# Kernel tuning notes

Measured on AMD Instinct MI355X. Metric: run time of the kernel, lower is better.

## Reference

```python
import jax, jax.numpy as jnp
import numpy as np

E = 800000
NUM_RADIAL = 6
HIDDEN = 128
OUT = 128
NUM_NODES = 50000


def setup_inputs() -> dict:
    key = jax.random.key(0)
    ks = jax.random.split(key, 12)
    x = jax.random.normal(ks[0], (E, HIDDEN), dtype=jnp.float32)
    rbf = jax.random.uniform(ks[1], (E, NUM_RADIAL), dtype=jnp.float32)
    i = jax.random.randint(ks[2], (E,), 0, NUM_NODES, dtype=jnp.int64)
    s = 1.0 / np.sqrt(HIDDEN)
    W_rbf = jax.random.normal(ks[3], (HIDDEN, NUM_RADIAL), dtype=jnp.float32) / np.sqrt(NUM_RADIAL)
    W1 = jax.random.normal(ks[4], (HIDDEN, HIDDEN), dtype=jnp.float32) * s
    b1 = jnp.zeros((HIDDEN,), dtype=jnp.float32)
    W2 = jax.random.normal(ks[5], (HIDDEN, HIDDEN), dtype=jnp.float32) * s
    b2 = jnp.zeros((HIDDEN,), dtype=jnp.float32)
    W3 = jax.random.normal(ks[6], (HIDDEN, HIDDEN), dtype=jnp.float32) * s
    b3 = jnp.zeros((HIDDEN,), dtype=jnp.float32)
    W_out = jax.random.normal(ks[7], (OUT, HIDDEN), dtype=jnp.float32) * s
    return {"x": x, "rbf": rbf, "i": i, "num_nodes": NUM_NODES,
            "W_rbf": W_rbf, "W1": W1, "b1": b1, "W2": W2, "b2": b2,
            "W3": W3, "b3": b3, "W_out": W_out}


def reference(x, rbf, i, num_nodes, W_rbf, W1, b1, W2, b2, W3, b3, W_out):
    # edge-wise: lin_rbf(rbf) * x, then scatter-add to nodes
    m = (rbf @ W_rbf.T) * x                      # [E, H]
    h = jax.ops.segment_sum(m, i, num_segments=num_nodes)  # [N, H]
    # MLP stack with swish activation
    h = jax.nn.silu(h @ W1.T + b1)
    h = jax.nn.silu(h @ W2.T + b2)
    h = jax.nn.silu(h @ W3.T + b3)
    return h @ W_out.T                           # [N, OUT]
```

## Files before the change

kernel.cpp:

```cpp
#include <hip/hip_runtime.h>
#include <hip/hip_bf16.h>

#define H 128
#define NR 6
#define MT 128
#define HS 136

typedef __attribute__((ext_vector_type(8))) short short8_t;
typedef __attribute__((ext_vector_type(4))) float f32x4;

__device__ __forceinline__ float silu_f(float v) {
    return v / (1.0f + __expf(-v));
}

__device__ __forceinline__ unsigned short bf16_rne(float f) {
    unsigned u = __float_as_uint(f);
    u += 0x7FFF + ((u >> 16) & 1);
    return (unsigned short)(u >> 16);
}
__device__ __forceinline__ float bf16_to_f(unsigned short s) {
    return __uint_as_float(((unsigned)s) << 16);
}

__global__ __launch_bounds__(256) void hist_k(const int* __restrict__ idx,
                                              int* __restrict__ counts, int E) {
    int i = blockIdx.x * 256 + threadIdx.x;
    if (i < E) atomicAdd(&counts[idx[i]], 1);
}

__global__ __launch_bounds__(1024) void scan_k(const int* __restrict__ counts,
                                               int* __restrict__ offsets, int N) {
    __shared__ int tmp[1024];
    const int tid = threadIdx.x;
    const int CHUNK = (N + 1023) >> 10;
    const int base = tid * CHUNK;
    int s = 0;
    for (int k = 0; k < CHUNK; ++k) {
        int j = base + k;
        if (j < N) s += counts[j];
    }
    tmp[tid] = s;
    __syncthreads();
    for (int off = 1; off < 1024; off <<= 1) {
        int v = (tid >= off) ? tmp[tid - off] : 0;
        __syncthreads();
        tmp[tid] += v;
        __syncthreads();
    }
    int run = tmp[tid] - s;
    for (int k = 0; k < CHUNK; ++k) {
        int j = base + k;
        if (j < N) { offsets[j] = run; run += counts[j]; }
    }
    if (tid == 1023) offsets[N] = run;
}

__global__ __launch_bounds__(256) void fill_k(const int* __restrict__ idx,
                                              const int* __restrict__ offsets,
                                              int* __restrict__ cursor,
                                              int* __restrict__ elist, int E) {
    int i = blockIdx.x * 256 + threadIdx.x;
    if (i < E) {
        int node = idx[i];
        int pos = atomicAdd(&cursor[node], 1);
        elist[offsets[node] + pos] = i;
    }
}

__global__ __launch_bounds__(256) void gather_k(
    const float* __restrict__ x, const float* __restrict__ rbf,
    const float* __restrict__ W_rbf,
    const int* __restrict__ offsets, const int* __restrict__ elist,
    float* __restrict__ h, int N)
{
    const int t = threadIdx.x;
    const int lane = t & 63;
    const int node = blockIdx.x * 4 + (t >> 6);
    if (node >= N) return;

    const float4* wp = (const float4*)(W_rbf + lane * 12);
    const float4 wa = wp[0], wb = wp[1], wc = wp[2];
    const float wr0[NR] = {wa.x, wa.y, wa.z, wa.w, wb.x, wb.y};
    const float wr1[NR] = {wb.z, wb.w, wc.x, wc.y, wc.z, wc.w};

    const int beg = offsets[node], end = offsets[node + 1];
    float ax = 0.f, ay = 0.f;

    int p = beg;
    for (; p + 1 < end; p += 2) {
        const int e0 = elist[p], e1 = elist[p + 1];
        const float2 xv0 = *(const float2*)(x + (size_t)e0 * H + lane * 2);
        const float2 xv1 = *(const float2*)(x + (size_t)e1 * H + lane * 2);
        const float* r0 = rbf + (size_t)e0 * NR;
        const float* r1 = rbf + (size_t)e1 * NR;
        float m0 = 0.f, m1 = 0.f, n0 = 0.f, n1 = 0.f;
        #pragma unroll
        for (int j = 0; j < NR; ++j) {
            m0 += r0[j] * wr0[j]; m1 += r0[j] * wr1[j];
            n0 += r1[j] * wr0[j]; n1 += r1[j] * wr1[j];
        }
        ax += m0 * xv0.x + n0 * xv1.x;
        ay += m1 * xv0.y + n1 * xv1.y;
    }
    if (p < end) {
        const int e0 = elist[p];
        const float2 xv0 = *(const float2*)(x + (size_t)e0 * H + lane * 2);
        const float* r0 = rbf + (size_t)e0 * NR;
        float m0 = 0.f, m1 = 0.f;
        #pragma unroll
        for (int j = 0; j < NR; ++j) { m0 += r0[j] * wr0[j]; m1 += r0[j] * wr1[j]; }
        ax += m0 * xv0.x;
        ay += m1 * xv0.y;
    }
    *(float2*)(h + (size_t)node * H + lane * 2) = make_float2(ax, ay);
}


__device__ __forceinline__ void stage_w_lds(const float* __restrict__ Wg,
        unsigned short* w_hi, unsigned short* w_lo, int t)
{
    for (int i = t * 4; i < H * H; i += 1024) {
        const float4 v = *(const float4*)(Wg + i);
        const int c = i >> 7, k = i & 127;
        ushort4 hi4, lo4;
        hi4.x = bf16_rne(v.x); lo4.x = bf16_rne(v.x - bf16_to_f(hi4.x));
        hi4.y = bf16_rne(v.y); lo4.y = bf16_rne(v.y - bf16_to_f(hi4.y));
        hi4.z = bf16_rne(v.z); lo4.z = bf16_rne(v.z - bf16_to_f(hi4.z));
        hi4.w = bf16_rne(v.w); lo4.w = bf16_rne(v.w - bf16_to_f(hi4.w));
        *(ushort4*)&w_hi[c * HS + k] = hi4;
        *(ushort4*)&w_lo[c * HS + k] = lo4;
    }
}

__device__ __forceinline__ void compute_gemm(
    const unsigned short* h_hi, const unsigned short* h_lo,
    const unsigned short* w_hi, const unsigned short* w_lo,
    const float* bl, int wv, int lr, int quad, f32x4 (&acc)[2][8])
{
    short8_t a_hi[2][4], a_lo[2][4];
    #pragma unroll
    for (int s = 0; s < 2; ++s) {
        const int row = (wv * 2 + s) * 16 + lr;
        #pragma unroll
        for (int kb = 0; kb < 4; ++kb) {
            const int off = row * HS + kb * 32 + quad * 8;
            a_hi[s][kb] = *(const short8_t*)&h_hi[off];
            a_lo[s][kb] = *(const short8_t*)&h_lo[off];
        }
    }
    #pragma unroll 2
    for (int ct = 0; ct < 8; ++ct) {
        const int c = ct * 16 + lr;
        const float b = bl[c];
        f32x4 acc0 = {b, b, b, b}, acc1 = {b, b, b, b};
        short8_t b_hi[4], b_lo[4];
        #pragma unroll
        for (int kb = 0; kb < 4; ++kb) {
            const int off = c * HS + kb * 32 + quad * 8;
            b_hi[kb] = *(const short8_t*)&w_hi[off];
            b_lo[kb] = *(const short8_t*)&w_lo[off];
        }
        #pragma unroll
        for (int kb = 0; kb < 4; ++kb) {
            acc0 = __builtin_amdgcn_mfma_f32_16x16x32_bf16(a_hi[0][kb], b_hi[kb], acc0, 0, 0, 0);
            acc1 = __builtin_amdgcn_mfma_f32_16x16x32_bf16(a_hi[1][kb], b_hi[kb], acc1, 0, 0, 0);
            acc0 = __builtin_amdgcn_mfma_f32_16x16x32_bf16(a_hi[0][kb], b_lo[kb], acc0, 0, 0, 0);
            acc1 = __builtin_amdgcn_mfma_f32_16x16x32_bf16(a_hi[1][kb], b_lo[kb], acc1, 0, 0, 0);
            acc0 = __builtin_amdgcn_mfma_f32_16x16x32_bf16(a_lo[0][kb], b_hi[kb], acc0, 0, 0, 0);
            acc1 = __builtin_amdgcn_mfma_f32_16x16x32_bf16(a_lo[1][kb], b_hi[kb], acc1, 0, 0, 0);
        }
        acc[0][ct] = acc0;
        acc[1][ct] = acc1;
    }
}

__device__ __forceinline__ void epilogue_silu(
    unsigned short* h_hi, unsigned short* h_lo,
    f32x4 (&acc)[2][8], int wv, int lr, int quad)
{
    #pragma unroll
    for (int s = 0; s < 2; ++s)
        #pragma unroll
        for (int ct = 0; ct < 8; ++ct)
            #pragma unroll
            for (int r = 0; r < 4; ++r) {
                const int row = (wv * 2 + s) * 16 + quad * 4 + r;
                const int col = ct * 16 + lr;
                const float v = silu_f(acc[s][ct][r]);
                const unsigned short hi = bf16_rne(v);
                h_hi[row * HS + col] = hi;
                h_lo[row * HS + col] = bf16_rne(v - bf16_to_f(hi));
            }
}

__global__ __launch_bounds__(256, 1) void mlp_mfma(
    const float* __restrict__ hg,
    const float* __restrict__ W1, const float* __restrict__ b1,
    const float* __restrict__ W2, const float* __restrict__ b2,
    const float* __restrict__ W3, const float* __restrict__ b3,
    const float* __restrict__ Wo,
    float* __restrict__ out, int N)
{
    __shared__ unsigned short h_hi[H * HS], h_lo[H * HS];
    __shared__ unsigned short w_hi[H * HS], w_lo[H * HS];
    __shared__ float bl[H];

    const int t = threadIdx.x;
    const int lane = t & 63;
    const int wv = t >> 6;
    const int lr = lane & 15;
    const int quad = lane >> 4;
    const int row0 = blockIdx.x * MT;

    for (int i = t * 4; i < MT * H; i += 1024) {
        const int r = i >> 7, k = i & 127;
        const int row = row0 + r;
        const float4 v = (row < N) ? *(const float4*)(hg + (size_t)row * H + k)
                                   : make_float4(0.f, 0.f, 0.f, 0.f);
        ushort4 hi4, lo4;
        hi4.x = bf16_rne(v.x); lo4.x = bf16_rne(v.x - bf16_to_f(hi4.x));
        hi4.y = bf16_rne(v.y); lo4.y = bf16_rne(v.y - bf16_to_f(hi4.y));
        hi4.z = bf16_rne(v.z); lo4.z = bf16_rne(v.z - bf16_to_f(hi4.z));
        hi4.w = bf16_rne(v.w); lo4.w = bf16_rne(v.w - bf16_to_f(hi4.w));
        *(ushort4*)&h_hi[r * HS + k] = hi4;
        *(ushort4*)&h_lo[r * HS + k] = lo4;
    }
    stage_w_lds(W1, w_hi, w_lo, t);
    if (t < H) bl[t] = b1[t];
    __syncthreads();

    f32x4 acc[2][8];

    compute_gemm(h_hi, h_lo, w_hi, w_lo, bl, wv, lr, quad, acc);
    __syncthreads();
    epilogue_silu(h_hi, h_lo, acc, wv, lr, quad);
    stage_w_lds(W2, w_hi, w_lo, t);
    if (t < H) bl[t] = b2[t];
    __syncthreads();

    compute_gemm(h_hi, h_lo, w_hi, w_lo, bl, wv, lr, quad, acc);
    __syncthreads();
    epilogue_silu(h_hi, h_lo, acc, wv, lr, quad);
    stage_w_lds(W3, w_hi, w_lo, t);
    if (t < H) bl[t] = b3[t];
    __syncthreads();

    compute_gemm(h_hi, h_lo, w_hi, w_lo, bl, wv, lr, quad, acc);
    __syncthreads();
    epilogue_silu(h_hi, h_lo, acc, wv, lr, quad);
    stage_w_lds(Wo, w_hi, w_lo, t);
    if (t < H) bl[t] = 0.f;
    __syncthreads();

    compute_gemm(h_hi, h_lo, w_hi, w_lo, bl, wv, lr, quad, acc);

    #pragma unroll
    for (int s = 0; s < 2; ++s)
        #pragma unroll
        for (int ct = 0; ct < 8; ++ct)
            #pragma unroll
            for (int r = 0; r < 4; ++r) {
                const int row = row0 + (wv * 2 + s) * 16 + quad * 4 + r;
                if (row < N) out[(size_t)row * H + ct * 16 + lr] = acc[s][ct][r];
            }
}

static inline size_t align256(size_t v) { return (v + 255) & ~(size_t)255; }

extern "C" void kernel_launch(void* const* d_in, const int* in_sizes, int n_in,
                              void* d_out, int out_size, void* d_ws, size_t ws_size,
                              hipStream_t stream) {
    const float* x     = (const float*)d_in[0];
    const float* rbf   = (const float*)d_in[1];
    const int*   idx   = (const int*)d_in[2];
    const float* W_rbf = (const float*)d_in[4];
    const float* W1    = (const float*)d_in[5];
    const float* b1    = (const float*)d_in[6];
    const float* W2    = (const float*)d_in[7];
    const float* b2    = (const float*)d_in[8];
    const float* W3    = (const float*)d_in[9];
    const float* b3    = (const float*)d_in[10];
    const float* Wo    = (const float*)d_in[11];
    float* out = (float*)d_out;

    const int E = in_sizes[0] / H;
    const int N = out_size / H;

    char* ws = (char*)d_ws;
    size_t off = 0;
    float* h       = (float*)(ws + off); off = align256(off + (size_t)N * H * 4);
    int*   counts  = (int*)(ws + off);   off = align256(off + (size_t)N * 4);
    int*   cursor  = (int*)(ws + off);   off = align256(off + (size_t)N * 4);
    int*   offsets = (int*)(ws + off);   off = align256(off + (size_t)(N + 1) * 4);
    int*   elist   = (int*)(ws + off);   off = align256(off + (size_t)E * 4);

    hipMemsetAsync(counts, 0, (char*)offsets - (char*)counts, stream);

    hist_k<<<(E + 255) / 256, 256, 0, stream>>>(idx, counts, E);
    scan_k<<<1, 1024, 0, stream>>>(counts, offsets, N);
    fill_k<<<(E + 255) / 256, 256, 0, stream>>>(idx, offsets, cursor, elist, E);
    gather_k<<<(N + 3) / 4, 256, 0, stream>>>(x, rbf, W_rbf, offsets, elist, h, N);
    mlp_mfma<<<(N + MT - 1) / MT, 256, 0, stream>>>(h, W1, b1, W2, b2, W3, b3, Wo, out, N);
}
```

Measured before the change: 889.4 us.

## Use wave-shuffle scan, batched edge gather, and 512-thread MLP blocks

Replaces the chunked serial-per-thread scan with a coalesced wave-shuffle block scan over 1024-element tiles. The gather kernel now loads 64 edge indices per wave at once, broadcasts them with shuffles, and issues four edges' x and rbf loads together to expose more memory-level parallelism. The MLP kernel doubles threads per block to 512 (one 16-row slab per wave) with launch bounds allowing two blocks per CU, trading per-wave register reuse of B fragments for higher occupancy.

Result: faster. 791.3 us (-11.0%).

```diff
diff --git a/kernel.cpp b/kernel.cpp
--- a/kernel.cpp
+++ b/kernel.cpp
@@ -30,29 +30,41 @@
 
 __global__ __launch_bounds__(1024) void scan_k(const int* __restrict__ counts,
                                                int* __restrict__ offsets, int N) {
-    __shared__ int tmp[1024];
-    const int tid = threadIdx.x;
-    const int CHUNK = (N + 1023) >> 10;
-    const int base = tid * CHUNK;
-    int s = 0;
-    for (int k = 0; k < CHUNK; ++k) {
-        int j = base + k;
-        if (j < N) s += counts[j];
-    }
-    tmp[tid] = s;
-    __syncthreads();
-    for (int off = 1; off < 1024; off <<= 1) {
-        int v = (tid >= off) ? tmp[tid - off] : 0;
+    __shared__ int wsum[16];
+    __shared__ int runv;
+    const int tid = threadIdx.x, lane = tid & 63, wv = tid >> 6;
+    if (tid == 0) runv = 0;
+    __syncthreads();
+    for (int base = 0; base < N; base += 1024) {
+        const int j = base + tid;
+        const int v_in = (j < N) ? counts[j] : 0;
+        int v = v_in;
+        #pragma unroll
+        for (int d = 1; d < 64; d <<= 1) {
+            int u = __shfl_up(v, d);
+            if (lane >= d) v += u;
+        }
+        if (lane == 63) wsum[wv] = v;
         __syncthreads();
-        tmp[tid] += v;
+        if (tid < 16) {
+            int s = wsum[tid];
+            #pragma unroll
+            for (int d = 1; d < 16; d <<= 1) {
+                int u = __shfl_up(s, d);
+                if (tid >= d) s += u;
+            }
+            wsum[tid] = s;
+        }
         __syncthreads();
-    }
-    int run = tmp[tid] - s;
-    for (int k = 0; k < CHUNK; ++k) {
-        int j = base + k;
-        if (j < N) { offsets[j] = run; run += counts[j]; }
-    }
-    if (tid == 1023) offsets[N] = run;
+        const int wexcl = (wv == 0) ? 0 : wsum[wv - 1];
+        const int r0 = runv;
+        if (j < N) offsets[j] = r0 + wexcl + (v - v_in);
+        const int tot = wsum[15];
+        __syncthreads();
+        if (tid == 0) runv = r0 + tot;
+        __syncthreads();
+    }
+    if (tid == 0) offsets[N] = runv;
 }
 
 __global__ __launch_bounds__(256) void fill_k(const int* __restrict__ idx,
@@ -86,31 +98,46 @@
     const int beg = offsets[node], end = offsets[node + 1];
     float ax = 0.f, ay = 0.f;
 
-    int p = beg;
-    for (; p + 1 < end; p += 2) {
-        const int e0 = elist[p], e1 = elist[p + 1];
-        const float2 xv0 = *(const float2*)(x + (size_t)e0 * H + lane * 2);
-        const float2 xv1 = *(const float2*)(x + (size_t)e1 * H + lane * 2);
-        const float* r0 = rbf + (size_t)e0 * NR;
-        const float* r1 = rbf + (size_t)e1 * NR;
-        float m0 = 0.f, m1 = 0.f, n0 = 0.f, n1 = 0.f;
-        #pragma unroll
-        for (int j = 0; j < NR; ++j) {
-            m0 += r0[j] * wr0[j]; m1 += r0[j] * wr1[j];
-            n0 += r1[j] * wr0[j]; n1 += r1[j] * wr1[j];
-        }
-        ax += m0 * xv0.x + n0 * xv1.x;
-        ay += m1 * xv0.y + n1 * xv1.y;
-    }
-    if (p < end) {
-        const int e0 = elist[p];
-        const float2 xv0 = *(const float2*)(x + (size_t)e0 * H + lane * 2);
-        const float* r0 = rbf + (size_t)e0 * NR;
-        float m0 = 0.f, m1 = 0.f;
-        #pragma unroll
-        for (int j = 0; j < NR; ++j) { m0 += r0[j] * wr0[j]; m1 += r0[j] * wr1[j]; }
-        ax += m0 * xv0.x;
-        ay += m1 * xv0.y;
+    for (int base = beg; base < end; base += 64) {
+        const int cnt = min(64, end - base);
+        const int e_lane = (lane < cnt) ? elist[base + lane] : 0;
+        int p = 0;
+        for (; p + 4 <= cnt; p += 4) {
+            int ev[4];
+            float2 xv[4];
+            float2 rv[4][3];
+            #pragma unroll
+            for (int q = 0; q < 4; ++q) ev[q] = __shfl(e_lane, p + q);
+            #pragma unroll
+            for (int q = 0; q < 4; ++q) {
+                const size_t e = (size_t)ev[q];
+                xv[q] = *(const float2*)(x + e * H + lane * 2);
+                const float2* rp = (const float2*)(rbf + e * NR);
+                rv[q][0] = rp[0]; rv[q][1] = rp[1]; rv[q][2] = rp[2];
+            }
+            #pragma unroll
+            for (int q = 0; q < 4; ++q) {
+                const float rr[NR] = {rv[q][0].x, rv[q][0].y, rv[q][1].x,
+                                      rv[q][1].y, rv[q][2].x, rv[q][2].y};
+                float m0 = 0.f, m1 = 0.f;
+                #pragma unroll
+                for (int j = 0; j < NR; ++j) { m0 += rr[j] * wr0[j]; m1 += rr[j] * wr1[j]; }
+                ax += m0 * xv[q].x;
+                ay += m1 * xv[q].y;
+            }
+        }
+        for (; p < cnt; ++p) {
+            const size_t e = (size_t)__shfl(e_lane, p);
+            const float2 xv0 = *(const float2*)(x + e * H + lane * 2);
+            const float2* rp = (const float2*)(rbf + e * NR);
+            const float2 ra = rp[0], rb2 = rp[1], rc2 = rp[2];
+            const float rr[NR] = {ra.x, ra.y, rb2.x, rb2.y, rc2.x, rc2.y};
+            float m0 = 0.f, m1 = 0.f;
+            #pragma unroll
+            for (int j = 0; j < NR; ++j) { m0 += rr[j] * wr0[j]; m1 += rr[j] * wr1[j]; }
+            ax += m0 * xv0.x;
+            ay += m1 * xv0.y;
+        }
     }
     *(float2*)(h + (size_t)node * H + lane * 2) = make_float2(ax, ay);
 }
@@ -119,7 +146,7 @@
 __device__ __forceinline__ void stage_w_lds(const float* __restrict__ Wg,
         unsigned short* w_hi, unsigned short* w_lo, int t)
 {
-    for (int i = t * 4; i < H * H; i += 1024) {
+    for (int i = t * 4; i < H * H; i += 2048) {
         const float4 v = *(const float4*)(Wg + i);
         const int c = i >> 7, k = i & 127;
         ushort4 hi4, lo4;
@@ -135,65 +162,63 @@
 __device__ __forceinline__ void compute_gemm(
     const unsigned short* h_hi, const unsigned short* h_lo,
     const unsigned short* w_hi, const unsigned short* w_lo,
-    const float* bl, int wv, int lr, int quad, f32x4 (&acc)[2][8])
-{
-    short8_t a_hi[2][4], a_lo[2][4];
+    const float* bl, int wv, int lr, int quad, f32x4 (&acc)[8])
+{
+    short8_t a_hi[4], a_lo[4];
+    const int row = wv * 16 + lr;
     #pragma unroll
-    for (int s = 0; s < 2; ++s) {
-        const int row = (wv * 2 + s) * 16 + lr;
+    for (int kb = 0; kb < 4; ++kb) {
+        const int off = row * HS + kb * 32 + quad * 8;
+        a_hi[kb] = *(const short8_t*)&h_hi[off];
+        a_lo[kb] = *(const short8_t*)&h_lo[off];
+    }
+    #pragma unroll
+    for (int ct = 0; ct < 8; ct += 2) {
+        const int c0 = ct * 16 + lr, c1 = (ct + 1) * 16 + lr;
+        const float bb0 = bl[c0], bb1 = bl[c1];
+        f32x4 A0 = {bb0, bb0, bb0, bb0}, A1 = {bb1, bb1, bb1, bb1};
+        short8_t b0h[4], b0l[4], b1h[4], b1l[4];
         #pragma unroll
         for (int kb = 0; kb < 4; ++kb) {
-            const int off = row * HS + kb * 32 + quad * 8;
-            a_hi[s][kb] = *(const short8_t*)&h_hi[off];
-            a_lo[s][kb] = *(const short8_t*)&h_lo[off];
-        }
-    }
-    #pragma unroll 2
-    for (int ct = 0; ct < 8; ++ct) {
-        const int c = ct * 16 + lr;
-        const float b = bl[c];
-        f32x4 acc0 = {b, b, b, b}, acc1 = {b, b, b, b};
-        short8_t b_hi[4], b_lo[4];
+            const int o0 = c0 * HS + kb * 32 + quad * 8;
+            const int o1 = c1 * HS + kb * 32 + quad * 8;
+            b0h[kb] = *(const short8_t*)&w_hi[o0];
+            b0l[kb] = *(const short8_t*)&w_lo[o0];
+            b1h[kb] = *(const short8_t*)&w_hi[o1];
+            b1l[kb] = *(const short8_t*)&w_lo[o1];
+        }
         #pragma unroll
         for (int kb = 0; kb < 4; ++kb) {
-            const int off = c * HS + kb * 32 + quad * 8;
-            b_hi[kb] = *(const short8_t*)&w_hi[off];
-            b_lo[kb] = *(const short8_t*)&w_lo[off];
-        }
-        #pragma unroll
-        for (int kb = 0; kb < 4; ++kb) {
-            acc0 = __builtin_amdgcn_mfma_f32_16x16x32_bf16(a_hi[0][kb], b_hi[kb], acc0, 0, 0, 0);
-            acc1 = __builtin_amdgcn_mfma_f32_16x16x32_bf16(a_hi[1][kb], b_hi[kb], acc1, 0, 0, 0);
-            acc0 = __builtin_amdgcn_mfma_f32_16x16x32_bf16(a_hi[0][kb], b_lo[kb], acc0, 0, 0, 0);
-            acc1 = __builtin_amdgcn_mfma_f32_16x16x32_bf16(a_hi[1][kb], b_lo[kb], acc1, 0, 0, 0);
-            acc0 = __builtin_amdgcn_mfma_f32_16x16x32_bf16(a_lo[0][kb], b_hi[kb], acc0, 0, 0, 0);
-            acc1 = __builtin_amdgcn_mfma_f32_16x16x32_bf16(a_lo[1][kb], b_hi[kb], acc1, 0, 0, 0);
-        }
-        acc[0][ct] = acc0;
-        acc[1][ct] = acc1;
+            A0 = __builtin_amdgcn_mfma_f32_16x16x32_bf16(a_hi[kb], b0h[kb], A0, 0, 0, 0);
+            A1 = __builtin_amdgcn_mfma_f32_16x16x32_bf16(a_hi[kb], b1h[kb], A1, 0, 0, 0);
+            A0 = __builtin_amdgcn_mfma_f32_16x16x32_bf16(a_hi[kb], b0l[kb], A0, 0, 0, 0);
+            A1 = __builtin_amdgcn_mfma_f32_16x16x32_bf16(a_hi[kb], b1l[kb], A1, 0, 0, 0);
+            A0 = __builtin_amdgcn_mfma_f32_16x16x32_bf16(a_lo[kb], b0h[kb], A0, 0, 0, 0);
+            A1 = __builtin_amdgcn_mfma_f32_16x16x32_bf16(a_lo[kb], b1h[kb], A1, 0, 0, 0);
+        }
+        acc[ct] = A0;
+        acc[ct + 1] = A1;
     }
 }
 
 __device__ __forceinline__ void epilogue_silu(
     unsigned short* h_hi, unsigned short* h_lo,
-    f32x4 (&acc)[2][8], int wv, int lr, int quad)
+    f32x4 (&acc)[8], int wv, int lr, int quad)
 {
     #pragma unroll
-    for (int s = 0; s < 2; ++s)
-        #pragma unroll
-        for (int ct = 0; ct < 8; ++ct)
-            #pragma unroll
-            for (int r = 0; r < 4; ++r) {
-                const int row = (wv * 2 + s) * 16 + quad * 4 + r;
-                const int col = ct * 16 + lr;
-                const float v = silu_f(acc[s][ct][r]);
-                const unsigned short hi = bf16_rne(v);
-                h_hi[row * HS + col] = hi;
-                h_lo[row * HS + col] = bf16_rne(v - bf16_to_f(hi));
-            }
-}
-
-__global__ __launch_bounds__(256, 1) void mlp_mfma(
+    for (int ct = 0; ct < 8; ++ct)
+        #pragma unroll
+        for (int r = 0; r < 4; ++r) {
+            const int row = wv * 16 + quad * 4 + r;
+            const int col = ct * 16 + lr;
+            const float v = silu_f(acc[ct][r]);
+            const unsigned short hi = bf16_rne(v);
+            h_hi[row * HS + col] = hi;
+            h_lo[row * HS + col] = bf16_rne(v - bf16_to_f(hi));
+        }
+}
+
+__global__ __launch_bounds__(512, 2) void mlp_mfma(
     const float* __restrict__ hg,
     const float* __restrict__ W1, const float* __restrict__ b1,
     const float* __restrict__ W2, const float* __restrict__ b2,
@@ -212,7 +237,7 @@
     const int quad = lane >> 4;
     const int row0 = blockIdx.x * MT;
 
-    for (int i = t * 4; i < MT * H; i += 1024) {
+    for (int i = t * 4; i < MT * H; i += 2048) {
         const int r = i >> 7, k = i & 127;
         const int row = row0 + r;
         const float4 v = (row < N) ? *(const float4*)(hg + (size_t)row * H + k)
@@ -229,7 +254,7 @@
     if (t < H) bl[t] = b1[t];
     __syncthreads();
 
-    f32x4 acc[2][8];
+    f32x4 acc[8];
 
     compute_gemm(h_hi, h_lo, w_hi, w_lo, bl, wv, lr, quad, acc);
     __syncthreads();
@@ -255,14 +280,12 @@
     compute_gemm(h_hi, h_lo, w_hi, w_lo, bl, wv, lr, quad, acc);
 
     #pragma unroll
-    for (int s = 0; s < 2; ++s)
-        #pragma unroll
-        for (int ct = 0; ct < 8; ++ct)
-            #pragma unroll
-            for (int r = 0; r < 4; ++r) {
-                const int row = row0 + (wv * 2 + s) * 16 + quad * 4 + r;
-                if (row < N) out[(size_t)row * H + ct * 16 + lr] = acc[s][ct][r];
-            }
+    for (int ct = 0; ct < 8; ++ct)
+        #pragma unroll
+        for (int r = 0; r < 4; ++r) {
+            const int row = row0 + wv * 16 + quad * 4 + r;
+            if (row < N) out[(size_t)row * H + ct * 16 + lr] = acc[ct][r];
+        }
 }
 
 static inline size_t align256(size_t v) { return (v + 255) & ~(size_t)255; }
@@ -300,5 +323,5 @@
     scan_k<<<1, 1024, 0, stream>>>(counts, offsets, N);
     fill_k<<<(E + 255) / 256, 256, 0, stream>>>(idx, offsets, cursor, elist, E);
     gather_k<<<(N + 3) / 4, 256, 0, stream>>>(x, rbf, W_rbf, offsets, elist, h, N);
-    mlp_mfma<<<(N + MT - 1) / MT, 256, 0, stream>>>(h, W1, b1, W2, b2, W3, b3, Wo, out, N);
-}
+    mlp_mfma<<<(N + MT - 1) / MT, 512, 0, stream>>>(h, W1, b1, W2, b2, W3, b3, Wo, out, N);
+}
```
